# Performance work log

Measured on AMD Instinct MI355X. Metric: run time of the kernel, lower is better.

The kernel has to match this reference:

```python
import jax, jax.numpy as jnp
import numpy as np

N, K, D = 524288, 64, 2
EPS = 1e-6
LOG_2PI = float(np.log(2.0 * np.pi))


def setup_inputs() -> dict:
    key = jax.random.key(0)
    k1, k2, k3, k4 = jax.random.split(key, 4)
    x = jax.random.normal(k1, (N, D), dtype=jnp.float32) * 2.0
    means = jax.random.normal(k2, (K, D), dtype=jnp.float32)
    # cholesky factor param: identity plus small noise (tril applied in forward)
    chol_var = jnp.eye(D, dtype=jnp.float32)[None] + 0.1 * jax.random.normal(k3, (K, D, D), dtype=jnp.float32)
    pi = jax.random.uniform(k4, (K,), dtype=jnp.float32)
    return {"x": x, "means": means, "chol_var": chol_var, "pi": pi}


def reference(x, means, chol_var, pi):
    # x: [N, D]; means: [K, D]; chol_var: [K, D, D]; pi: [K]
    K_, D_ = means.shape
    L = jnp.tril(chol_var)                                   # [K, D, D]
    cov = L @ jnp.swapaxes(L, -1, -2) + EPS * jnp.eye(D_, dtype=x.dtype)
    chol = jnp.linalg.cholesky(cov)                          # [K, D, D] lower
    logdet = 2.0 * jnp.sum(jnp.log(jnp.diagonal(chol, axis1=-2, axis2=-1)), axis=-1)  # [K]
    cinv = jnp.linalg.inv(chol)                              # [K, D, D] (tiny DxD)
    diff = x[:, None, :] - means[None, :, :]                 # [N, K, D]
    y = jnp.einsum('kij,nkj->nki', cinv, diff)               # whitened residuals
    quad = jnp.sum(y * y, axis=-1)                           # [N, K] Mahalanobis^2
    log_probs = -0.5 * (D_ * LOG_2PI + logdet[None, :] + quad)  # [N, K]
    weighted = log_probs + jax.nn.log_softmax(pi)            # [N, K]
    return jax.nn.logsumexp(weighted, axis=1)                # [N]
```

## Files before the change

kernel.cpp:

```cpp
#include <hip/hip_runtime.h>
#include <hip/hip_bf16.h>
#include <math.h>
#include <stdint.h>

#define K_COMP 64
#define LOG_2PI_D 1.837877066409345483560659472811
#define LOG2E_D   1.442695040888963407359924681002
#define LN2_F     0.69314718055994530942f

__global__ void gmm_setup(const float* __restrict__ means,
                          const float* __restrict__ chol_var,
                          const float* __restrict__ pi,
                          float* __restrict__ coef) {
    int k = threadIdx.x;

    float p = pi[k];
    float mx = p;
    #pragma unroll
    for (int off = 32; off > 0; off >>= 1) mx = fmaxf(mx, __shfl_xor(mx, off, 64));
    float ef = __expf(p - mx);
    float sf = ef;
    #pragma unroll
    for (int off = 32; off > 0; off >>= 1) sf += __shfl_xor(sf, off, 64);
    double logpi = (double)p - (double)mx - (double)__logf(sf);

    double v00 = (double)chol_var[k*4 + 0];
    double v10 = (double)chol_var[k*4 + 2];
    double v11 = (double)chol_var[k*4 + 3];
    const double eps = 1e-6;
    double cov00 = v00*v00 + eps;
    double cov01 = v00*v10;
    double cov11 = v10*v10 + v11*v11 + eps;

    double a = sqrt(cov00);
    double b = cov01 / a;
    double c2 = cov11 - b*b;
    double c = sqrt(c2);
    double logdet = (double)__logf((float)(cov00 * c2));

    double P00 = 1.0/cov00 + (b*b)/(cov00*c2);
    double P01 = -b/(a*c2);
    double P11 = 1.0/c2;

    double m0 = (double)means[k*2 + 0];
    double m1 = (double)means[k*2 + 1];

    double constk = -0.5*(2.0*LOG_2PI_D + logdet) + logpi;

    coef[k*6 + 0] = (float)(-0.5*P00*LOG2E_D);
    coef[k*6 + 1] = (float)(-P01*LOG2E_D);
    coef[k*6 + 2] = (float)(-0.5*P11*LOG2E_D);
    coef[k*6 + 3] = (float)((P00*m0 + P01*m1)*LOG2E_D);
    coef[k*6 + 4] = (float)((P01*m0 + P11*m1)*LOG2E_D);
    coef[k*6 + 5] = (float)((constk
                     - 0.5*(P00*m0*m0 + 2.0*P01*m0*m1 + P11*m1*m1))*LOG2E_D);
}

typedef const float __attribute__((address_space(4))) cfloat;

__global__ __launch_bounds__(256) void gmm_main(const float* __restrict__ x,
                                                const float* __restrict__ coef,
                                                float* __restrict__ out,
                                                int n) {
    int i = blockIdx.x * 256 + threadIdx.x;
    if (i >= n) return;

    cfloat* cc = (cfloat*)(uintptr_t)coef;

    float2 xv = reinterpret_cast<const float2*>(x)[i];
    float x0 = xv.x, x1 = xv.y;
    float x00 = x0*x0, x01 = x0*x1, x11 = x1*x1;

    float w[K_COMP];
    float m = -INFINITY;
    #pragma unroll
    for (int k = 0; k < K_COMP; ++k) {
        float t = cc[k*6 + 5];
        t = fmaf(cc[k*6 + 0], x00, t);
        t = fmaf(cc[k*6 + 1], x01, t);
        t = fmaf(cc[k*6 + 2], x11, t);
        t = fmaf(cc[k*6 + 3], x0,  t);
        t = fmaf(cc[k*6 + 4], x1,  t);
        w[k] = t;
        m = fmaxf(m, t);
    }

    float s0 = 0.f, s1 = 0.f, s2 = 0.f, s3 = 0.f;
    #pragma unroll
    for (int k = 0; k < K_COMP; k += 4) {
        s0 += __builtin_amdgcn_exp2f(w[k]     - m);
        s1 += __builtin_amdgcn_exp2f(w[k + 1] - m);
        s2 += __builtin_amdgcn_exp2f(w[k + 2] - m);
        s3 += __builtin_amdgcn_exp2f(w[k + 3] - m);
    }
    float s = (s0 + s1) + (s2 + s3);

    out[i] = LN2_F * (m + __builtin_amdgcn_logf(s));
}

extern "C" void kernel_launch(void* const* d_in, const int* in_sizes, int n_in,
                              void* d_out, int out_size, void* d_ws, size_t ws_size,
                              hipStream_t stream) {
    const float* x        = (const float*)d_in[0];
    const float* means    = (const float*)d_in[1];
    const float* chol_var = (const float*)d_in[2];
    const float* pi       = (const float*)d_in[3];
    float* out  = (float*)d_out;
    float* coef = (float*)d_ws;

    int n = in_sizes[0] / 2;

    gmm_setup<<<1, 64, 0, stream>>>(means, chol_var, pi, coef);
    gmm_main<<<(n + 255) / 256, 256, 0, stream>>>(x, coef, out, n);
}
```

Before: 69.50 us.

## Fuse coefficient setup into main kernel and process two points per thread

Removes the separate one-block setup launch: every block recomputes the 64 component coefficients into its own scratch slice, then reads them back through scalar constant loads after a fence and barrier. Each thread now handles two points using float4 loads and float2 stores, so every coefficient load is reused twice. The cost is redundant per-block setup work in double precision, more scratch memory, twice the register pressure (128 live values), and a possible tail bug when n is odd.

```diff
diff --git a/kernel.cpp b/kernel.cpp
--- a/kernel.cpp
+++ b/kernel.cpp
@@ -3,99 +3,103 @@
 #include <math.h>
 #include <stdint.h>
 
-#define K_COMP 64
 #define LOG_2PI_D 1.837877066409345483560659472811
 #define LOG2E_D   1.442695040888963407359924681002
 #define LN2_F     0.69314718055994530942f
 
-__global__ void gmm_setup(const float* __restrict__ means,
-                          const float* __restrict__ chol_var,
-                          const float* __restrict__ pi,
-                          float* __restrict__ coef) {
-    int k = threadIdx.x;
-
-    float p = pi[k];
-    float mx = p;
-    #pragma unroll
-    for (int off = 32; off > 0; off >>= 1) mx = fmaxf(mx, __shfl_xor(mx, off, 64));
-    float ef = __expf(p - mx);
-    float sf = ef;
-    #pragma unroll
-    for (int off = 32; off > 0; off >>= 1) sf += __shfl_xor(sf, off, 64);
-    double logpi = (double)p - (double)mx - (double)__logf(sf);
-
-    double v00 = (double)chol_var[k*4 + 0];
-    double v10 = (double)chol_var[k*4 + 2];
-    double v11 = (double)chol_var[k*4 + 3];
-    const double eps = 1e-6;
-    double cov00 = v00*v00 + eps;
-    double cov01 = v00*v10;
-    double cov11 = v10*v10 + v11*v11 + eps;
-
-    double a = sqrt(cov00);
-    double b = cov01 / a;
-    double c2 = cov11 - b*b;
-    double c = sqrt(c2);
-    double logdet = (double)__logf((float)(cov00 * c2));
-
-    double P00 = 1.0/cov00 + (b*b)/(cov00*c2);
-    double P01 = -b/(a*c2);
-    double P11 = 1.0/c2;
-
-    double m0 = (double)means[k*2 + 0];
-    double m1 = (double)means[k*2 + 1];
-
-    double constk = -0.5*(2.0*LOG_2PI_D + logdet) + logpi;
-
-    coef[k*6 + 0] = (float)(-0.5*P00*LOG2E_D);
-    coef[k*6 + 1] = (float)(-P01*LOG2E_D);
-    coef[k*6 + 2] = (float)(-0.5*P11*LOG2E_D);
-    coef[k*6 + 3] = (float)((P00*m0 + P01*m1)*LOG2E_D);
-    coef[k*6 + 4] = (float)((P01*m0 + P11*m1)*LOG2E_D);
-    coef[k*6 + 5] = (float)((constk
-                     - 0.5*(P00*m0*m0 + 2.0*P01*m0*m1 + P11*m1*m1))*LOG2E_D);
-}
-
 typedef const float __attribute__((address_space(4))) cfloat;
 
-__global__ __launch_bounds__(256) void gmm_main(const float* __restrict__ x,
-                                                const float* __restrict__ coef,
-                                                float* __restrict__ out,
-                                                int n) {
-    int i = blockIdx.x * 256 + threadIdx.x;
-    if (i >= n) return;
+__global__ __launch_bounds__(256) void gmm_fused(
+        const float* __restrict__ x,
+        const float* __restrict__ means,
+        const float* __restrict__ chol_var,
+        const float* __restrict__ pi,
+        float* __restrict__ out,
+        float* __restrict__ scratch,
+        int n2) {
+    const int tid = threadIdx.x;
+    const int bid = blockIdx.x;
+    float* my = scratch + (size_t)bid * 384;
 
-    cfloat* cc = (cfloat*)(uintptr_t)coef;
+    if (tid < 64) {
+        const int k = tid;
+        float p = pi[k];
+        float mx = p;
+        #pragma unroll
+        for (int off = 32; off > 0; off >>= 1) mx = fmaxf(mx, __shfl_xor(mx, off, 64));
+        float sf = __expf(p - mx);
+        #pragma unroll
+        for (int off = 32; off > 0; off >>= 1) sf += __shfl_xor(sf, off, 64);
+        double logpi = (double)p - (double)mx - (double)__logf(sf);
 
-    float2 xv = reinterpret_cast<const float2*>(x)[i];
-    float x0 = xv.x, x1 = xv.y;
-    float x00 = x0*x0, x01 = x0*x1, x11 = x1*x1;
+        double v00 = (double)chol_var[k*4 + 0];
+        double v10 = (double)chol_var[k*4 + 2];
+        double v11 = (double)chol_var[k*4 + 3];
+        const double eps = 1e-6;
+        double cov00 = v00*v00 + eps;
+        double cov01 = v00*v10;
+        double cov11 = v10*v10 + v11*v11 + eps;
+        double a  = sqrt(cov00);
+        double b  = cov01 / a;
+        double c2 = cov11 - b*b;
+        double logdet = (double)__logf((float)(cov00 * c2));
+        double P00 = 1.0/cov00 + (b*b)/(cov00*c2);
+        double P01 = -b/(a*c2);
+        double P11 = 1.0/c2;
+        double m0 = (double)means[k*2 + 0];
+        double m1 = (double)means[k*2 + 1];
+        double constk = -0.5*(2.0*LOG_2PI_D + logdet) + logpi;
 
-    float w[K_COMP];
-    float m = -INFINITY;
+        my[k*6 + 0] = (float)(-0.5*P00*LOG2E_D);
+        my[k*6 + 1] = (float)(-P01*LOG2E_D);
+        my[k*6 + 2] = (float)(-0.5*P11*LOG2E_D);
+        my[k*6 + 3] = (float)((P00*m0 + P01*m1)*LOG2E_D);
+        my[k*6 + 4] = (float)((P01*m0 + P11*m1)*LOG2E_D);
+        my[k*6 + 5] = (float)((constk
+                        - 0.5*(P00*m0*m0 + 2.0*P01*m0*m1 + P11*m1*m1))*LOG2E_D);
+        __threadfence();
+    }
+    __syncthreads();
+
+    const float* cp = my;
+    asm volatile("" : "+s"(cp) :: "memory");
+    cfloat* cc = (cfloat*)(uintptr_t)cp;
+
+    int i = bid * 256 + tid;
+    if (i >= n2) return;
+
+    float4 xv = reinterpret_cast<const float4*>(x)[i];
+    float a00 = xv.x*xv.x, a01 = xv.x*xv.y, a11 = xv.y*xv.y;
+    float b00 = xv.z*xv.z, b01 = xv.z*xv.w, b11 = xv.w*xv.w;
+
+    float wa[64], wb[64];
+    float ma = -INFINITY, mb = -INFINITY;
     #pragma unroll
-    for (int k = 0; k < K_COMP; ++k) {
-        float t = cc[k*6 + 5];
-        t = fmaf(cc[k*6 + 0], x00, t);
-        t = fmaf(cc[k*6 + 1], x01, t);
-        t = fmaf(cc[k*6 + 2], x11, t);
-        t = fmaf(cc[k*6 + 3], x0,  t);
-        t = fmaf(cc[k*6 + 4], x1,  t);
-        w[k] = t;
-        m = fmaxf(m, t);
+    for (int k = 0; k < 64; ++k) {
+        float C0 = cc[k*6+0], C1 = cc[k*6+1], C2 = cc[k*6+2];
+        float C3 = cc[k*6+3], C4 = cc[k*6+4], C5 = cc[k*6+5];
+        float ta = C5, tb = C5;
+        ta = fmaf(C0, a00, ta);   tb = fmaf(C0, b00, tb);
+        ta = fmaf(C1, a01, ta);   tb = fmaf(C1, b01, tb);
+        ta = fmaf(C2, a11, ta);   tb = fmaf(C2, b11, tb);
+        ta = fmaf(C3, xv.x, ta);  tb = fmaf(C3, xv.z, tb);
+        ta = fmaf(C4, xv.y, ta);  tb = fmaf(C4, xv.w, tb);
+        wa[k] = ta;  wb[k] = tb;
+        ma = fmaxf(ma, ta);  mb = fmaxf(mb, tb);
     }
 
-    float s0 = 0.f, s1 = 0.f, s2 = 0.f, s3 = 0.f;
+    float sa0 = 0.f, sa1 = 0.f, sb0 = 0.f, sb1 = 0.f;
     #pragma unroll
-    for (int k = 0; k < K_COMP; k += 4) {
-        s0 += __builtin_amdgcn_exp2f(w[k]     - m);
-        s1 += __builtin_amdgcn_exp2f(w[k + 1] - m);
-        s2 += __builtin_amdgcn_exp2f(w[k + 2] - m);
-        s3 += __builtin_amdgcn_exp2f(w[k + 3] - m);
+    for (int k = 0; k < 64; k += 2) {
+        sa0 += __builtin_amdgcn_exp2f(wa[k]   - ma);
+        sa1 += __builtin_amdgcn_exp2f(wa[k+1] - ma);
+        sb0 += __builtin_amdgcn_exp2f(wb[k]   - mb);
+        sb1 += __builtin_amdgcn_exp2f(wb[k+1] - mb);
     }
-    float s = (s0 + s1) + (s2 + s3);
-
-    out[i] = LN2_F * (m + __builtin_amdgcn_logf(s));
+    float2 o;
+    o.x = LN2_F * (ma + __builtin_amdgcn_logf(sa0 + sa1));
+    o.y = LN2_F * (mb + __builtin_amdgcn_logf(sb0 + sb1));
+    reinterpret_cast<float2*>(out)[i] = o;
 }
 
 extern "C" void kernel_launch(void* const* d_in, const int* in_sizes, int n_in,
@@ -105,11 +109,12 @@
     const float* means    = (const float*)d_in[1];
     const float* chol_var = (const float*)d_in[2];
     const float* pi       = (const float*)d_in[3];
-    float* out  = (float*)d_out;
-    float* coef = (float*)d_ws;
+    float* out     = (float*)d_out;
+    float* scratch = (float*)d_ws;
 
-    int n = in_sizes[0] / 2;
+    int n  = in_sizes[0] / 2;
+    int n2 = n / 2;
+    int blocks = (n2 + 255) / 256;
 
-    gmm_setup<<<1, 64, 0, stream>>>(means, chol_var, pi, coef);
-    gmm_main<<<(n + 255) / 256, 256, 0, stream>>>(x, coef, out, n);
+    gmm_fused<<<blocks, 256, 0, stream>>>(x, means, chol_var, pi, out, scratch, n2);
 }
```

Measured after the change: 103.6 us. 49.1% more time.
